# Kernel tuning notes

Hardware: AMD Instinct MI355X
Metric: run time of the kernel (lower is better)

## Reference

```python
import jax, jax.numpy as jnp
import numpy as np

N_NODES = 100000
N_EDGES = 400000
N_GRAPHS = 4096
D = 300          # emb_dim
L = 5            # num_layers
NUM_ATOM, NUM_CHIR = 120, 3
NUM_BOND, NUM_DIR = 6, 3
SELF_LOOP_BOND = 4
TEMP = 0.04


def setup_inputs() -> dict:
    key = jax.random.key(0)
    ks = jax.random.split(key, 24)
    inp = {}
    # graph batch 0
    inp["x0"] = jax.random.randint(ks[0], (N_NODES, 2), 0, 3)
    inp["edge_index0"] = jax.random.randint(ks[1], (2, N_EDGES), 0, N_NODES)
    inp["edge_attr0"] = jax.random.randint(ks[2], (N_EDGES, 2), 0, 3)
    inp["batch_ids0"] = jnp.sort(jax.random.randint(ks[3], (N_NODES,), 0, N_GRAPHS))
    inp["dangling0"] = jax.random.randint(ks[4], (N_GRAPHS,), 0, N_NODES)
    # graph batch 1
    inp["x1"] = jax.random.randint(ks[5], (N_NODES, 2), 0, 3)
    inp["edge_index1"] = jax.random.randint(ks[6], (2, N_EDGES), 0, N_NODES)
    inp["edge_attr1"] = jax.random.randint(ks[7], (N_EDGES, 2), 0, 3)
    inp["batch_ids1"] = jnp.sort(jax.random.randint(ks[8], (N_NODES,), 0, N_GRAPHS))
    inp["dangling1"] = jax.random.randint(ks[9], (N_GRAPHS,), 0, N_NODES)
    # shared encoder parameters
    g = lambda i, shp, s=0.1: (jax.random.normal(ks[i], shp, jnp.float32) * s)
    inp["atom_emb1"] = g(10, (NUM_ATOM, D))
    inp["atom_emb2"] = g(11, (NUM_CHIR, D))
    inp["eemb1"] = g(12, (L, NUM_BOND, D))
    inp["eemb2"] = g(13, (L, NUM_DIR, D))
    inp["W1"] = g(14, (L, D, 2 * D))
    inp["b1"] = jnp.zeros((L, 2 * D), jnp.float32)
    inp["W2"] = g(15, (L, 2 * D, D))
    inp["b2"] = jnp.zeros((L, D), jnp.float32)
    inp["bn_g"] = jnp.ones((L, D), jnp.float32)
    inp["bn_b"] = jnp.zeros((L, D), jnp.float32)
    # projectors stacked: 0=projector0, 1=projector1, 2=dangling_proj0, 3=dangling_proj1
    inp["pW1"] = g(16, (4, D, D))
    inp["pb1"] = jnp.zeros((4, D), jnp.float32)
    inp["pW2"] = g(17, (4, D, D))
    inp["pb2"] = jnp.zeros((4, D), jnp.float32)
    return inp


def _encode(x, edge_index, edge_attr, atom_emb1, atom_emb2,
            eemb1, eemb2, W1, b1, W2, b2, bn_g, bn_b):
    # initial node embedding: sum of atom-type and chirality embeddings
    h = atom_emb1[x[:, 0]] + atom_emb2[x[:, 1]]          # [N, D]
    src, dst = edge_index[0], edge_index[1]
    for l in range(L):
        e = eemb1[l][edge_attr[:, 0]] + eemb2[l][edge_attr[:, 1]]  # [E, D]
        msg = h[src] + e                                           # [E, D]
        agg = jax.ops.segment_sum(msg, dst, num_segments=h.shape[0])
        # self-loop with bond type 4, direction 0 (pretrain-gnns GINConv)
        agg = agg + h + eemb1[l][SELF_LOOP_BOND] + eemb2[l][0]
        z = jax.nn.relu(agg @ W1[l] + b1[l]) @ W2[l] + b2[l]       # GIN MLP
        mu = jnp.mean(z, axis=0)
        var = jnp.var(z, axis=0)
        z = (z - mu) * jax.lax.rsqrt(var + 1e-5) * bn_g[l] + bn_b[l]
        h = z if l == L - 1 else jax.nn.relu(z)                    # no ReLU on last layer
    return h


def _mlp(x, w1, bb1, w2, bb2):
    return jax.nn.relu(x @ w1 + bb1) @ w2 + bb2


def _branch(h, batch_ids, dangling, proj_i, dproj_i, pW1, pb1, pW2, pb2):
    pooled = jax.ops.segment_sum(h, batch_ids, num_segments=N_GRAPHS)
    counts = jax.ops.segment_sum(jnp.ones((h.shape[0],), h.dtype), batch_ids,
                                 num_segments=N_GRAPHS)
    pooled = pooled / jnp.maximum(counts, 1.0)[:, None]            # global_mean_pool
    out = _mlp(pooled, pW1[proj_i], pb1[proj_i], pW2[proj_i], pb2[proj_i])
    out = out + _mlp(h[dangling], pW1[dproj_i], pb1[dproj_i], pW2[dproj_i], pb2[dproj_i])
    return out / jnp.linalg.norm(out, axis=1, keepdims=True)       # L2 normalize


def reference(x0, edge_index0, edge_attr0, batch_ids0, dangling0,
              x1, edge_index1, edge_attr1, batch_ids1, dangling1,
              atom_emb1, atom_emb2, eemb1, eemb2, W1, b1, W2, b2, bn_g, bn_b,
              pW1, pb1, pW2, pb2):
    h0 = _encode(x0, edge_index0, edge_attr0, atom_emb1, atom_emb2,
                 eemb1, eemb2, W1, b1, W2, b2, bn_g, bn_b)
    f0 = _branch(h0, batch_ids0, dangling0, 0, 2, pW1, pb1, pW2, pb2)
    h1 = _encode(x1, edge_index1, edge_attr1, atom_emb1, atom_emb2,
                 eemb1, eemb2, W1, b1, W2, b2, bn_g, bn_b)
    f1 = _branch(h1, batch_ids1, dangling1, 1, 3, pW1, pb1, pW2, pb2)
    logits = (f0 @ f1.T) / TEMP                                    # [G, G]
    return logits
```

## Files before the change

kernel.cpp:

```cpp
#include <hip/hip_runtime.h>

#define NN    100000
#define NE    400000
#define NG    4096
#define LL    5
#define MPAD  100096
#define NCHUNK 98

typedef unsigned short u16;
typedef __attribute__((ext_vector_type(8))) _Float16 half8;
typedef __attribute__((ext_vector_type(4))) float float4v;

__device__ __forceinline__ float b2f(u16 u){
  union { float f; unsigned u; } c; c.u = ((unsigned)u)<<16; return c.f;
}
__device__ __forceinline__ u16 f2b(float f){
  union { float f; unsigned u; } c; c.f = f;
  unsigned x = c.u;
  return (u16)((x + 0x7fffu + ((x>>16)&1u)) >> 16);
}
__device__ __forceinline__ float h2f(u16 u){
  union { u16 s; _Float16 h; } c; c.s = u; return (float)c.h;
}
__device__ __forceinline__ u16 f2h(float f){
  union { u16 s; _Float16 h; } c; c.h = (_Float16)f; return c.s;
}
__device__ __forceinline__ void g2l16(const u16* g, u16* l){
  __builtin_amdgcn_global_load_lds((const __attribute__((address_space(1))) void*)g,
                                   (__attribute__((address_space(3))) void*)l, 16, 0, 0);
}

__global__ __launch_bounds__(256) void detect_dtype(const u16* __restrict__ p, int* __restrict__ flag){
  int i = blockIdx.x*256 + threadIdx.x;
  float v = b2f(p[i]);
  if (!(fabsf(v) <= 1e4f)) atomicOr(flag, 1);
}
__global__ __launch_bounds__(256) void cvt_param(const void* __restrict__ src, u16* __restrict__ dst,
                                                 int n, const int* __restrict__ flag){
  int i = blockIdx.x*256 + threadIdx.x;
  if (i >= n) return;
  float v = (*flag) ? ((const float*)src)[i] : b2f(((const u16*)src)[i]);
  dst[i] = f2h(v);
}

__global__ __launch_bounds__(256) void zero32(unsigned* __restrict__ p, int n){
  int i = blockIdx.x*256 + threadIdx.x;
  if (i < n) p[i] = 0u;
}

__global__ __launch_bounds__(256) void tpad(const u16* __restrict__ src, u16* __restrict__ dst,
                                            int L, int K, int N, int Kp, int Np){
  int idx = blockIdx.x*256 + threadIdx.x;
  if (idx >= L*Np*Kp) return;
  int l = idx/(Np*Kp); int r = idx - l*Np*Kp; int n = r/Kp; int k = r - n*Kp;
  dst[idx] = (n<N && k<K) ? src[(l*K + k)*N + n] : (u16)0;
}

__global__ __launch_bounds__(256) void ecomb_build(const u16* __restrict__ ee1, const u16* __restrict__ ee2,
                                                   u16* __restrict__ ec){
  int idx = blockIdx.x*256 + threadIdx.x;
  if (idx >= LL*18*160) return;
  int l = idx/(18*160); int r = idx - l*18*160; int c = r/160; int p = r - c*160;
  int a0 = c/3, a1 = c - a0*3;
  u16 o0=0,o1=0;
  if (p < 150){
    int d = 2*p;
    o0 = f2h(h2f(ee1[(l*6+a0)*300+d  ]) + h2f(ee2[(l*3+a1)*300+d  ]));
    o1 = f2h(h2f(ee1[(l*6+a0)*300+d+1]) + h2f(ee2[(l*3+a1)*300+d+1]));
  }
  ((ushort2*)ec)[idx] = make_ushort2(o0,o1);
}

__global__ __launch_bounds__(256) void node_init(const int* __restrict__ x, const u16* __restrict__ ae1,
                                                 const u16* __restrict__ ae2, u16* __restrict__ h){
  int idx = blockIdx.x*256 + threadIdx.x;
  if (idx >= MPAD*160) return;
  int n = idx/160, p = idx - n*160;
  u16 o0=0,o1=0;
  if (n < NN && p < 150){
    int a = x[2*n], ch = x[2*n+1];
    int d = 2*p;
    o0 = f2h(h2f(ae1[a*300+d  ]) + h2f(ae2[ch*300+d  ]));
    o1 = f2h(h2f(ae1[a*300+d+1]) + h2f(ae2[ch*300+d+1]));
  }
  ((ushort2*)h)[idx] = make_ushort2(o0,o1);
}

__global__ __launch_bounds__(256) void hist(const int* __restrict__ ei, int* __restrict__ counts){
  int e = blockIdx.x*256 + threadIdx.x;
  if (e >= NE) return;
  atomicAdd(&counts[ei[NE + e]], 1);
}
__global__ __launch_bounds__(256) void scan_chunks(const int* __restrict__ counts, int* __restrict__ csums){
  __shared__ int sd[256];
  int base = blockIdx.x*1024;
  int s = 0;
  for (int i = threadIdx.x; i < 1024; i += 256){ int g = base+i; if (g < NN) s += counts[g]; }
  sd[threadIdx.x] = s; __syncthreads();
  for (int off=128; off>0; off>>=1){ if (threadIdx.x < off) sd[threadIdx.x] += sd[threadIdx.x+off]; __syncthreads(); }
  if (threadIdx.x == 0) csums[blockIdx.x] = sd[0];
}
__global__ __launch_bounds__(128) void scan_base(const int* __restrict__ csums, int* __restrict__ cbase,
                                                 int* __restrict__ offsets){
  __shared__ int sd[128];
  int tid = threadIdx.x;
  int v = (tid < NCHUNK) ? csums[tid] : 0;
  sd[tid] = v; __syncthreads();
  for (int off=1; off<128; off<<=1){
    int t = (tid >= off) ? sd[tid-off] : 0; __syncthreads();
    sd[tid] += t; __syncthreads();
  }
  if (tid < NCHUNK) cbase[tid] = sd[tid] - v;
  if (tid == 0) offsets[NN] = sd[NCHUNK-1];
}
__global__ __launch_bounds__(256) void scan_final(const int* __restrict__ counts, const int* __restrict__ cbase,
                                                  int* __restrict__ offsets){
  __shared__ int sd[256];
  int tid = threadIdx.x;
  int base = blockIdx.x*1024 + tid*4;
  int v0 = (base   < NN) ? counts[base  ] : 0;
  int v1 = (base+1 < NN) ? counts[base+1] : 0;
  int v2 = (base+2 < NN) ? counts[base+2] : 0;
  int v3 = (base+3 < NN) ? counts[base+3] : 0;
  int s = v0+v1+v2+v3;
  sd[tid] = s; __syncthreads();
  for (int off=1; off<256; off<<=1){
    int t = (tid >= off) ? sd[tid-off] : 0; __syncthreads();
    sd[tid] += t; __syncthreads();
  }
  int run = cbase[blockIdx.x] + sd[tid] - s;
  if (base   < NN){ offsets[base  ] = run; } run += v0;
  if (base+1 < NN){ offsets[base+1] = run; } run += v1;
  if (base+2 < NN){ offsets[base+2] = run; } run += v2;
  if (base+3 < NN){ offsets[base+3] = run; }
}
__global__ __launch_bounds__(256) void fill_perm(const int* __restrict__ ei, const int* __restrict__ ea,
                                                 const int* __restrict__ offsets,
                                                 int* __restrict__ cursor, int* __restrict__ pk){
  int e = blockIdx.x*256 + threadIdx.x;
  if (e >= NE) return;
  int d = ei[NE + e];
  int src = ei[e];
  int c = ea[2*e]*3 + ea[2*e+1];
  int pos = offsets[d] + atomicAdd(&cursor[d], 1);
  pk[pos] = src*32 + c;
}

__global__ __launch_bounds__(256) void aggregate(
    const u16* __restrict__ h, const u16* __restrict__ ecL,
    const int* __restrict__ offsets, const int* __restrict__ pk,
    u16* __restrict__ agg)
{
  __shared__ u16 ecs[18*320];
  for (int i = threadIdx.x; i < 18*160; i += 256)
    ((ushort2*)ecs)[i] = ((const ushort2*)ecL)[i];
  __syncthreads();
  int node = blockIdx.x*4 + (threadIdx.x>>6);
  int lane = threadIdx.x & 63;
  bool tl = lane < 16;
  const ushort4* h4 = (const ushort4*)h;
  long base = (long)node*80;
  float m0[4], m1[4] = {0,0,0,0};
  {
    ushort4 hv = h4[base + lane];
    ushort4 ev = ((const ushort4*)(ecs + 12*320))[lane];
    m0[0]=h2f(hv.x)+h2f(ev.x); m0[1]=h2f(hv.y)+h2f(ev.y);
    m0[2]=h2f(hv.z)+h2f(ev.z); m0[3]=h2f(hv.w)+h2f(ev.w);
    if (tl){
      ushort4 hv2 = h4[base + 64 + lane];
      ushort4 ev2 = ((const ushort4*)(ecs + 12*320))[64 + lane];
      m1[0]=h2f(hv2.x)+h2f(ev2.x); m1[1]=h2f(hv2.y)+h2f(ev2.y);
      m1[2]=h2f(hv2.z)+h2f(ev2.z); m1[3]=h2f(hv2.w)+h2f(ev2.w);
    }
  }
  if (node < NN){
    int s = offsets[node], en = offsets[node+1];
    int i = s;
    while (i + 1 < en){
      int p0 = pk[i], p1 = pk[i+1]; i += 2;
      int s0 = p0>>5, c0 = p0&31;
      int s1 = p1>>5, c1 = p1&31;
      ushort4 ha0 = h4[(long)s0*80 + lane];
      ushort4 ha1 = h4[(long)s1*80 + lane];
      ushort4 e0 = ((const ushort4*)(ecs + c0*320))[lane];
      ushort4 e1 = ((const ushort4*)(ecs + c1*320))[lane];
      m0[0] += h2f(ha0.x)+h2f(e0.x) + h2f(ha1.x)+h2f(e1.x);
      m0[1] += h2f(ha0.y)+h2f(e0.y) + h2f(ha1.y)+h2f(e1.y);
      m0[2] += h2f(ha0.z)+h2f(e0.z) + h2f(ha1.z)+h2f(e1.z);
      m0[3] += h2f(ha0.w)+h2f(e0.w) + h2f(ha1.w)+h2f(e1.w);
      if (tl){
        ushort4 hb0 = h4[(long)s0*80 + 64 + lane];
        ushort4 hb1 = h4[(long)s1*80 + 64 + lane];
        ushort4 f0 = ((const ushort4*)(ecs + c0*320))[64 + lane];
        ushort4 f1 = ((const ushort4*)(ecs + c1*320))[64 + lane];
        m1[0] += h2f(hb0.x)+h2f(f0.x) + h2f(hb1.x)+h2f(f1.x);
        m1[1] += h2f(hb0.y)+h2f(f0.y) + h2f(hb1.y)+h2f(f1.y);
        m1[2] += h2f(hb0.z)+h2f(f0.z) + h2f(hb1.z)+h2f(f1.z);
        m1[3] += h2f(hb0.w)+h2f(f0.w) + h2f(hb1.w)+h2f(f1.w);
      }
    }
    if (i < en){
      int p0 = pk[i];
      int s0 = p0>>5, c0 = p0&31;
      ushort4 ha0 = h4[(long)s0*80 + lane];
      ushort4 e0 = ((const ushort4*)(ecs + c0*320))[lane];
      m0[0] += h2f(ha0.x)+h2f(e0.x); m0[1] += h2f(ha0.y)+h2f(e0.y);
      m0[2] += h2f(ha0.z)+h2f(e0.z); m0[3] += h2f(ha0.w)+h2f(e0.w);
      if (tl){
        ushort4 hb0 = h4[(long)s0*80 + 64 + lane];
        ushort4 f0 = ((const ushort4*)(ecs + c0*320))[64 + lane];
        m1[0] += h2f(hb0.x)+h2f(f0.x); m1[1] += h2f(hb0.y)+h2f(f0.y);
        m1[2] += h2f(hb0.z)+h2f(f0.z); m1[3] += h2f(hb0.w)+h2f(f0.w);
      }
    }
  }
  ushort4* a4 = (ushort4*)agg;
  a4[base + lane] = make_ushort4(f2h(m0[0]), f2h(m0[1]), f2h(m0[2]), f2h(m0[3]));
  if (tl)
    a4[base + 64 + lane] = make_ushort4(f2h(m1[0]), f2h(m1[1]), f2h(m1[2]), f2h(m1[3]));
}

__global__ __launch_bounds__(512, 2) void gin_mlp(
    const u16* __restrict__ A,
    const u16* __restrict__ W1Tl,
    const u16* __restrict__ b1l,
    const u16* __restrict__ W2Tl,
    const u16* __restrict__ b2l,
    u16* __restrict__ Z,
    float* __restrict__ colsum, float* __restrict__ colsumsq)
{
  __shared__ __align__(16) u16 lds[32768];
  u16* uS = lds;
  u16* Ws = lds + 8192;
  int tid = threadIdx.x;
  int wave = tid>>6, lane = tid&63;
  int q = lane>>4, r = lane&15;
  int wr = wave>>2, wc = wave&3;
  int m0 = blockIdx.x*128;

  half8 aReg[10];
  const u16* Arow = A + (long)(m0 + wave*16 + r)*320 + q*8;
  #pragma unroll
  for (int kc=0; kc<10; ++kc) aReg[kc] = *(const half8*)(Arow + kc*32);

  float4v zacc[4][6];
  #pragma unroll
  for (int i=0;i<4;i++)
    #pragma unroll
    for (int j=0;j<6;j++) zacc[i][j] = (float4v){0.f,0.f,0.f,0.f};

  for (int t1=0; t1<10; ++t1){
    int n1_0 = t1*64;
    __syncthreads();
    #pragma unroll
    for (int i=0;i<5;i++){
      int idx = tid*8 + i*4096;
      int kc = idx >> 11;
      int rem = idx & 2047;
      int n = rem >> 5, k8 = rem & 31;
      g2l16(W1Tl + (long)(n1_0 + n)*320 + kc*32 + k8, Ws + idx);
    }
    __syncthreads();
    float4v uacc[4];
    #pragma unroll
    for (int j=0;j<4;j++) uacc[j] = (float4v){0.f,0.f,0.f,0.f};
    #pragma unroll
    for (int kc=0; kc<10; ++kc){
      half8 bw[4];
      #pragma unroll
      for (int j=0;j<4;j++) bw[j] = *(const half8*)&Ws[kc*2048 + (j*16+r)*32 + q*8];
      #pragma unroll
      for (int j=0;j<4;j++)
        uacc[j] = __builtin_amdgcn_mfma_f32_16x16x32_f16(aReg[kc], bw[j], uacc[j], 0,0,0);
    }
    #pragma unroll
    for (int j=0;j<4;j++){
      int nloc = j*16 + r;
      int n1g = n1_0 + nloc;
      float bv = (n1g < 600) ? h2f(b1l[n1g]) : 0.f;
      int kc2 = nloc >> 5, c32 = nloc & 31;
      #pragma unroll
      for (int t=0;t<4;t++){
        int row = wave*16 + q*4 + t;
        float v = fmaxf(uacc[j][t] + bv, 0.f);
        uS[kc2*4096 + row*32 + c32] = f2h(v);
      }
    }
    __syncthreads();
    #pragma unroll
    for (int i=0;i<6;i++){
      int idx = tid*8 + i*4096;
      int kc2 = idx / 12288;
      int rem = idx - kc2*12288;
      int n2 = rem >> 5, k8 = rem & 31;
      g2l16(W2Tl + (long)n2*640 + n1_0 + kc2*32 + k8, Ws + idx);
    }
    __syncthreads();
    #pragma unroll
    for (int kc2=0; kc2<2; ++kc2){
      half8 af[4], bf[6];
      #pragma unroll
      for (int i=0;i<4;i++) af[i] = *(const half8*)&uS[kc2*4096 + (wr*64+i*16+r)*32 + q*8];
      #pragma unroll
      for (int j=0;j<6;j++) bf[j] = *(const half8*)&Ws[kc2*12288 + (wc*96+j*16+r)*32 + q*8];
      #pragma unroll
      for (int i=0;i<4;i++)
        #pragma unroll
        for (int j=0;j<6;j++)
          zacc[i][j] = __builtin_amdgcn_mfma_f32_16x16x32_f16(af[i], bf[j], zacc[i][j], 0,0,0);
    }
  }
  #pragma unroll
  for (int j=0;j<6;j++){
    int c = wc*96 + j*16 + r;
    float bv = (c < 300) ? h2f(b2l[c]) : 0.f;
    float s1 = 0.f, s2 = 0.f;
    #pragma unroll
    for (int i=0;i<4;i++){
      int rowb = m0 + wr*64 + i*16 + q*4;
      #pragma unroll
      for (int t=0;t<4;t++){
        float v = zacc[i][j][t] + bv;
        int gr = rowb + t;
        if (c < 320) Z[(long)gr*320 + c] = f2h(v);
        if (gr < NN){ s1 += v; s2 += v*v; }
      }
    }
    s1 += __shfl_xor(s1,16); s1 += __shfl_xor(s1,32);
    s2 += __shfl_xor(s2,16); s2 += __shfl_xor(s2,32);
    if (q == 0 && c < 384){ atomicAdd(&colsum[c], s1); atomicAdd(&colsumsq[c], s2); }
  }
}

__global__ __launch_bounds__(256) void gemm_nt(
    const u16* __restrict__ A, int lda,
    const u16* __restrict__ BT, int ldb,
    int Kp,
    const u16* __restrict__ bias, int Nreal,
    float scale, int dorelu, int omode, int Ncap,
    void* __restrict__ Cv, int ldc,
    const int* __restrict__ outmode)
{
  __shared__ __align__(16) u16 As[128*32];
  __shared__ __align__(16) u16 Bs[128*32];
  int tid = threadIdx.x;
  int wave = tid>>6, lane = tid&63;
  int wr = (wave>>1)&1, wc = wave&1;
  int m0 = blockIdx.x*128, n0 = blockIdx.y*128;
  int q = lane>>4, r = lane&15;
  int srow = tid>>2, scol = (tid&3)*8;
  const u16* Ag0 = A  + (long)(m0+srow)*lda + scol;
  const u16* Ag1 = A  + (long)(m0+64+srow)*lda + scol;
  const u16* Bg0 = BT + (long)(n0+srow)*ldb + scol;
  const u16* Bg1 = BT + (long)(n0+64+srow)*ldb + scol;
  u16* Asl0 = &As[tid*8];
  u16* Asl1 = &As[64*32 + tid*8];
  u16* Bsl0 = &Bs[tid*8];
  u16* Bsl1 = &Bs[64*32 + tid*8];
  float4v acc[4][4];
  #pragma unroll
  for (int i=0;i<4;i++)
    #pragma unroll
    for (int j=0;j<4;j++) acc[i][j] = (float4v){0.f,0.f,0.f,0.f};

  for (int k0=0; k0<Kp; k0+=32){
    g2l16(Ag0+k0, Asl0);
    g2l16(Ag1+k0, Asl1);
    g2l16(Bg0+k0, Bsl0);
    g2l16(Bg1+k0, Bsl1);
    __syncthreads();
    half8 af[4], bf[4];
    #pragma unroll
    for (int i=0;i<4;i++) af[i] = *(const half8*)&As[(wr*64+i*16+r)*32 + q*8];
    #pragma unroll
    for (int j=0;j<4;j++) bf[j] = *(const half8*)&Bs[(wc*64+j*16+r)*32 + q*8];
    #pragma unroll
    for (int i=0;i<4;i++)
      #pragma unroll
      for (int j=0;j<4;j++)
        acc[i][j] = __builtin_amdgcn_mfma_f32_16x16x32_f16(af[i], bf[j], acc[i][j], 0,0,0);
    __syncthreads();
  }

  int ob = omode;
  if (outmode) ob = (*outmode) ? 0 : 1;
  u16* Ch = (u16*)Cv; float* Cf = (float*)Cv;
  #pragma unroll
  for (int j=0;j<4;j++){
    int c = n0 + wc*64 + j*16 + r;
    float bv = (bias && c < Nreal) ? h2f(bias[c]) : 0.f;
    #pragma unroll
    for (int i=0;i<4;i++){
      int rowb = m0 + wr*64 + i*16 + q*4;
      #pragma unroll
      for (int tt=0; tt<4; ++tt){
        float v = acc[i][j][tt] + bv;
        if (dorelu) v = fmaxf(v, 0.f);
        v *= scale;
        int gr = rowb + tt;
        if (c < Ncap){
          long o = (long)gr*ldc + c;
          if (ob == 2)      Ch[o] = f2h(v);
          else if (ob == 1) Ch[o] = f2b(v);
          else              Cf[o] = v;
        }
      }
    }
  }
}

__global__ __launch_bounds__(320) void bn_finalize(const float* __restrict__ st, const u16* __restrict__ g,
                                                   const u16* __restrict__ b, float* __restrict__ sc,
                                                   float* __restrict__ sh){
  int c = threadIdx.x;
  if (c >= 300) return;
  float mu  = st[c] * (1.0f/NN);
  float var = st[384+c] * (1.0f/NN) - mu*mu;
  float inv = rsqrtf(var + 1e-5f);
  float gg = h2f(g[c]) * inv;
  sc[c] = gg; sh[c] = h2f(b[c]) - mu*gg;
}
__global__ __launch_bounds__(256) void bn_apply(const u16* __restrict__ z, const float* __restrict__ sc,
                                                const float* __restrict__ sh, u16* __restrict__ h, int dorelu){
  int idx = blockIdx.x*256 + threadIdx.x;
  if (idx >= NN*150) return;
  int n = idx/150, p = idx - n*150;
  ushort2 zz = ((const ushort2*)z)[n*160 + p];
  int d = 2*p;
  float v0 = h2f(zz.x)*sc[d  ] + sh[d  ];
  float v1 = h2f(zz.y)*sc[d+1] + sh[d+1];
  if (dorelu){ v0 = fmaxf(v0,0.f); v1 = fmaxf(v1,0.f); }
  ((ushort2*)h)[n*160 + p] = make_ushort2(f2h(v0), f2h(v1));
}

__global__ __launch_bounds__(256) void graph_starts(const int* __restrict__ ids, int* __restrict__ starts){
  int i = blockIdx.x*256 + threadIdx.x;
  if (i >= NN) return;
  int b = ids[i];
  if (i == 0){ for (int g=0; g<=b; ++g) starts[g] = 0; }
  else { int p = ids[i-1]; for (int g=p+1; g<=b; ++g) starts[g] = i; }
  if (i == NN-1){ for (int g=b+1; g<=NG; ++g) starts[g] = NN; }
}
__global__ __launch_bounds__(256) void pool_kernel(const u16* __restrict__ h, const int* __restrict__ starts,
                                                   u16* __restrict__ pooled){
  int g = blockIdx.x*4 + (threadIdx.x>>6);
  int lane = threadIdx.x & 63;
  if (g >= NG) return;
  int s = starts[g], e = starts[g+1];
  int cnt = e - s; if (cnt < 1) cnt = 1;
  float inv = 1.0f/(float)cnt;
  float ax[3] = {0,0,0}, ay[3] = {0,0,0};
  const ushort2* h2 = (const ushort2*)h;
  for (int row=s; row<e; ++row){
    long base = (long)row*160;
    #pragma unroll
    for (int jp=0; jp<3; ++jp){
      int p = jp*64 + lane;
      if (p < 160){ ushort2 v = h2[base+p]; ax[jp] += h2f(v.x); ay[jp] += h2f(v.y); }
    }
  }
  ushort2* o2 = (ushort2*)pooled;
  #pragma unroll
  for (int jp=0; jp<3; ++jp){
    int p = jp*64 + lane;
    if (p < 160) o2[g*160+p] = make_ushort2(f2h(ax[jp]*inv), f2h(ay[jp]*inv));
  }
}
__global__ __launch_bounds__(256) void gather_rows(const u16* __restrict__ h, const int* __restrict__ idxs,
                                                   u16* __restrict__ out){
  int idx = blockIdx.x*256 + threadIdx.x;
  if (idx >= NG*160) return;
  int g = idx/160, p = idx - g*160;
  ((ushort2*)out)[idx] = ((const ushort2*)h)[(long)idxs[g]*160 + p];
}
__global__ __launch_bounds__(256) void add_norm(const float* __restrict__ vp, const float* __restrict__ vd,
                                                u16* __restrict__ f){
  int g = blockIdx.x*4 + (threadIdx.x>>6);
  int lane = threadIdx.x & 63;
  if (g >= NG) return;
  float vals[5]; float ss = 0.f;
  #pragma unroll
  for (int t=0; t<5; ++t){
    int d = lane + 64*t; float v = 0.f;
    if (d < 300) v = vp[g*320+d] + vd[g*320+d];
    vals[t] = v; ss += v*v;
  }
  #pragma unroll
  for (int off=32; off>0; off>>=1) ss += __shfl_xor(ss, off);
  float inv = rsqrtf(ss);
  #pragma unroll
  for (int t=0; t<5; ++t){
    int d = lane + 64*t;
    if (d < 320) f[g*320+d] = f2h(d < 300 ? vals[t]*inv : 0.f);
  }
}

extern "C" void kernel_launch(void* const* d_in, const int* in_sizes, int n_in,
                              void* d_out, int out_size, void* d_ws, size_t ws_size,
                              hipStream_t stream)
{
  const int* xin[2]  = {(const int*)d_in[0], (const int*)d_in[5]};
  const int* ei[2]   = {(const int*)d_in[1], (const int*)d_in[6]};
  const int* ea[2]   = {(const int*)d_in[2], (const int*)d_in[7]};
  const int* bid[2]  = {(const int*)d_in[3], (const int*)d_in[8]};
  const int* dang[2] = {(const int*)d_in[4], (const int*)d_in[9]};
  (void)in_sizes; (void)n_in; (void)out_size; (void)ws_size;

  char* w = (char*)d_ws;
  auto alloc = [&](size_t bytes)->char* {
    char* p = w; w += (bytes + 255) & ~(size_t)255; return p;
  };
  u16* hA   = (u16*)alloc((size_t)MPAD*320*2);
  u16* agg  = (u16*)alloc((size_t)MPAD*320*2);
  u16* z    = agg;
  u16*   pooled = (u16*)alloc((size_t)NG*320*2);
  u16*   hd     = (u16*)alloc((size_t)NG*320*2);
  u16*   ubuf   = (u16*)alloc((size_t)NG*384*2);
  float* vpb    = (float*)alloc((size_t)NG*320*4);
  float* vdb    = (float*)alloc((size_t)NG*320*4);
  u16* ec   = (u16*)alloc((size_t)LL*18*320*2);
  u16* W1T  = (u16*)alloc((size_t)LL*640*320*2);
  u16* W2T  = (u16*)alloc((size_t)LL*384*640*2);
  u16* pW1T = (u16*)alloc((size_t)4*384*320*2);
  u16* pW2T = (u16*)alloc((size_t)4*384*384*2);
  int* counts = (int*)alloc((size_t)NN*4);
  int* cursor = (int*)alloc((size_t)NN*4);
  int* offs   = (int*)alloc((size_t)(NN+1)*4);
  int* perm   = (int*)alloc((size_t)NE*4);
  int* csums  = (int*)alloc(512);
  int* cbase  = (int*)alloc(512);
  float* stats = (float*)alloc(768*4);
  float* bnsc  = (float*)alloc(384*4);
  float* bnsh  = (float*)alloc(384*4);
  int* starts  = (int*)alloc((size_t)(NG+1)*4);
  u16* f0b     = (u16*)alloc((size_t)NG*320*2);
  u16* f1b     = (u16*)alloc((size_t)NG*320*2);
  int* dflag   = (int*)alloc(256);
  const int pcnt[14] = {36000, 900, 9000, 4500, 900000, 3000, 900000, 1500,
                        1500, 1500, 360000, 1200, 360000, 1200};
  u16* parena = (u16*)alloc((size_t)2580300*2 + 14*256);
  u16* pp[14];
  { size_t off = 0;
    for (int i=0;i<14;i++){ pp[i] = parena + off; off += (size_t)((pcnt[i]+127)&~127); } }
  u16* ae1 = pp[0];  u16* ae2 = pp[1];  u16* ee1 = pp[2];  u16* ee2 = pp[3];
  u16* W1  = pp[4];  u16* b1  = pp[5];  u16* W2  = pp[6];  u16* b2  = pp[7];
  u16* bng = pp[8];  u16* bnb = pp[9];  u16* pW1 = pp[10]; u16* pb1 = pp[11];
  u16* pW2 = pp[12]; u16* pb2 = pp[13];

  auto cdiv = [](long a, long b){ return (int)((a + b - 1)/b); };
  auto gemm = [&](const u16* A, int lda, const u16* BT, int ldb, int Kp,
                  const u16* bias, int Nreal, float scale, int relu, int omode, int Ncap,
                  void* C, int ldc, int gx, int gy, const int* om){
    gemm_nt<<<dim3(gx,gy), 256, 0, stream>>>(A,lda,BT,ldb,Kp,bias,Nreal,scale,relu,omode,Ncap,
                                             C,ldc,om);
  };

  zero32<<<1,256,0,stream>>>((unsigned*)dflag, 1);
  detect_dtype<<<16,256,0,stream>>>((const u16*)d_in[14], dflag);
  for (int i=0;i<14;i++)
    cvt_param<<<cdiv(pcnt[i],256),256,0,stream>>>(d_in[10+i], pp[i], pcnt[i], dflag);

  tpad<<<cdiv((long)LL*640*320,256),256,0,stream>>>(W1,  W1T,  LL, 300, 600, 320, 640);
  tpad<<<cdiv((long)LL*384*640,256),256,0,stream>>>(W2,  W2T,  LL, 600, 300, 640, 384);
  tpad<<<cdiv((long)4*384*320,256),256,0,stream>>>(pW1, pW1T, 4,  300, 300, 320, 384);
  tpad<<<cdiv((long)4*384*384,256),256,0,stream>>>(pW2, pW2T, 4,  300, 300, 384, 384);
  ecomb_build<<<cdiv((long)LL*18*160,256),256,0,stream>>>(ee1, ee2, ec);

  for (int br=0; br<2; ++br){
    u16* fo = br ? f1b : f0b;
    node_init<<<cdiv((long)MPAD*160,256),256,0,stream>>>(xin[br], ae1, ae2, hA);
    zero32<<<cdiv(NN,256),256,0,stream>>>((unsigned*)counts, NN);
    hist<<<cdiv(NE,256),256,0,stream>>>(ei[br], counts);
    scan_chunks<<<NCHUNK,256,0,stream>>>(counts, csums);
    scan_base<<<1,128,0,stream>>>(csums, cbase, offs);
    scan_final<<<NCHUNK,256,0,stream>>>(counts, cbase, offs);
    zero32<<<cdiv(NN,256),256,0,stream>>>((unsigned*)cursor, NN);
    fill_perm<<<cdiv(NE,256),256,0,stream>>>(ei[br], ea[br], offs, cursor, perm);

    for (int l=0; l<LL; ++l){
      aggregate<<<MPAD/4,256,0,stream>>>(hA, ec + (size_t)l*18*320, offs, perm, agg);
      zero32<<<3,256,0,stream>>>((unsigned*)stats, 768);
      gin_mlp<<<MPAD/128, 512, 0, stream>>>(agg,
          W1T + (size_t)l*640*320, b1 + l*600,
          W2T + (size_t)l*384*640, b2 + l*300,
          z, stats, stats+384);
      bn_finalize<<<1,320,0,stream>>>(stats, bng + l*300, bnb + l*300, bnsc, bnsh);
      bn_apply<<<cdiv((long)NN*150,256),256,0,stream>>>(z, bnsc, bnsh, hA, (l < LL-1) ? 1 : 0);
    }

    graph_starts<<<cdiv(NN,256),256,0,stream>>>(bid[br], starts);
    pool_kernel<<<NG/4,256,0,stream>>>(hA, starts, pooled);
    gather_rows<<<cdiv((long)NG*160,256),256,0,stream>>>(hA, dang[br], hd);

    int pi = br, dpi = 2 + br;
    gemm(pooled, 320, pW1T + (size_t)pi*384*320, 320, 320,
         pb1 + pi*300, 300, 1.f, 1, 2, 384, ubuf, 384, NG/128, 3, nullptr);
    gemm(ubuf, 384, pW2T + (size_t)pi*384*384, 384, 384,
         pb2 + pi*300, 300, 1.f, 0, 0, 320, vpb, 320, NG/128, 3, nullptr);
    gemm(hd, 320, pW1T + (size_t)dpi*384*320, 320, 320,
         pb1 + dpi*300, 300, 1.f, 1, 2, 384, ubuf, 384, NG/128, 3, nullptr);
    gemm(ubuf, 384, pW2T + (size_t)dpi*384*384, 384, 384,
         pb2 + dpi*300, 300, 1.f, 0, 0, 320, vdb, 320, NG/128, 3, nullptr);
    add_norm<<<NG/4,256,0,stream>>>(vpb, vdb, fo);
  }

  gemm(f0b, 320, f1b, 320, 320, nullptr, 0, 25.0f, 0, 1, NG,
       d_out, NG, NG/128, NG/128, dflag);
}
```

Measured before the change: 4.013 ms.

## Use packed fp16 accumulation in aggregate and 32x32 MFMA for first GIN layer

The aggregate kernel now accumulates neighbor messages directly in packed half4 vectors, with the edge loop unrolled by four, instead of converting each value to float. The first GEMM in gin_mlp switches from 16x16x32 MFMA tiles to 32x32x16 tiles, using a padded LDS layout (stride 328) for W1 to avoid bank conflicts and a new output-to-LDS mapping. The goal is less conversion ALU work and more memory-level parallelism in the gather, plus fewer LDS reads per MFMA in the GEMM. Accumulating sums in fp16 loses precision and risks overflow on high-degree nodes, and holding 20 A fragments raises register pressure.

```diff
diff --git a/kernel.cpp b/kernel.cpp
--- a/kernel.cpp
+++ b/kernel.cpp
@@ -9,7 +9,9 @@
 
 typedef unsigned short u16;
 typedef __attribute__((ext_vector_type(8))) _Float16 half8;
+typedef __attribute__((ext_vector_type(4))) _Float16 hv4;
 typedef __attribute__((ext_vector_type(4))) float float4v;
+typedef __attribute__((ext_vector_type(16))) float float16v;
 
 __device__ __forceinline__ float b2f(u16 u){
   union { float f; unsigned u; } c; c.u = ((unsigned)u)<<16; return c.f;
@@ -158,66 +160,41 @@
   int node = blockIdx.x*4 + (threadIdx.x>>6);
   int lane = threadIdx.x & 63;
   bool tl = lane < 16;
-  const ushort4* h4 = (const ushort4*)h;
+  const hv4* h4 = (const hv4*)h;
+  const hv4* e4 = (const hv4*)ecs;
   long base = (long)node*80;
-  float m0[4], m1[4] = {0,0,0,0};
-  {
-    ushort4 hv = h4[base + lane];
-    ushort4 ev = ((const ushort4*)(ecs + 12*320))[lane];
-    m0[0]=h2f(hv.x)+h2f(ev.x); m0[1]=h2f(hv.y)+h2f(ev.y);
-    m0[2]=h2f(hv.z)+h2f(ev.z); m0[3]=h2f(hv.w)+h2f(ev.w);
-    if (tl){
-      ushort4 hv2 = h4[base + 64 + lane];
-      ushort4 ev2 = ((const ushort4*)(ecs + 12*320))[64 + lane];
-      m1[0]=h2f(hv2.x)+h2f(ev2.x); m1[1]=h2f(hv2.y)+h2f(ev2.y);
-      m1[2]=h2f(hv2.z)+h2f(ev2.z); m1[3]=h2f(hv2.w)+h2f(ev2.w);
-    }
-  }
+  hv4 acc0, acc1 = (hv4)(_Float16)0;
+  acc0 = h4[base + lane] + e4[12*80 + lane];
+  if (tl) acc1 = h4[base + 64 + lane] + e4[12*80 + 64 + lane];
   if (node < NN){
     int s = offsets[node], en = offsets[node+1];
     int i = s;
-    while (i + 1 < en){
-      int p0 = pk[i], p1 = pk[i+1]; i += 2;
-      int s0 = p0>>5, c0 = p0&31;
-      int s1 = p1>>5, c1 = p1&31;
-      ushort4 ha0 = h4[(long)s0*80 + lane];
-      ushort4 ha1 = h4[(long)s1*80 + lane];
-      ushort4 e0 = ((const ushort4*)(ecs + c0*320))[lane];
-      ushort4 e1 = ((const ushort4*)(ecs + c1*320))[lane];
-      m0[0] += h2f(ha0.x)+h2f(e0.x) + h2f(ha1.x)+h2f(e1.x);
-      m0[1] += h2f(ha0.y)+h2f(e0.y) + h2f(ha1.y)+h2f(e1.y);
-      m0[2] += h2f(ha0.z)+h2f(e0.z) + h2f(ha1.z)+h2f(e1.z);
-      m0[3] += h2f(ha0.w)+h2f(e0.w) + h2f(ha1.w)+h2f(e1.w);
+    while (i + 3 < en){
+      int p0 = pk[i], p1 = pk[i+1], p2 = pk[i+2], p3 = pk[i+3]; i += 4;
+      long b0 = (long)(p0>>5)*80, b1 = (long)(p1>>5)*80;
+      long b2 = (long)(p2>>5)*80, b3 = (long)(p3>>5)*80;
+      int c0 = (p0&31)*80, c1 = (p1&31)*80, c2 = (p2&31)*80, c3 = (p3&31)*80;
+      hv4 a0 = h4[b0+lane], a1 = h4[b1+lane], a2 = h4[b2+lane], a3 = h4[b3+lane];
+      hv4 e0 = e4[c0+lane], e1 = e4[c1+lane], e2 = e4[c2+lane], e3 = e4[c3+lane];
+      acc0 += (a0+e0); acc0 += (a1+e1); acc0 += (a2+e2); acc0 += (a3+e3);
       if (tl){
-        ushort4 hb0 = h4[(long)s0*80 + 64 + lane];
-        ushort4 hb1 = h4[(long)s1*80 + 64 + lane];
-        ushort4 f0 = ((const ushort4*)(ecs + c0*320))[64 + lane];
-        ushort4 f1 = ((const ushort4*)(ecs + c1*320))[64 + lane];
-        m1[0] += h2f(hb0.x)+h2f(f0.x) + h2f(hb1.x)+h2f(f1.x);
-        m1[1] += h2f(hb0.y)+h2f(f0.y) + h2f(hb1.y)+h2f(f1.y);
-        m1[2] += h2f(hb0.z)+h2f(f0.z) + h2f(hb1.z)+h2f(f1.z);
-        m1[3] += h2f(hb0.w)+h2f(f0.w) + h2f(hb1.w)+h2f(f1.w);
+        hv4 x0 = h4[b0+64+lane], x1 = h4[b1+64+lane];
+        hv4 x2 = h4[b2+64+lane], x3 = h4[b3+64+lane];
+        hv4 y0 = e4[c0+64+lane], y1 = e4[c1+64+lane];
+        hv4 y2 = e4[c2+64+lane], y3 = e4[c3+64+lane];
+        acc1 += (x0+y0); acc1 += (x1+y1); acc1 += (x2+y2); acc1 += (x3+y3);
       }
     }
-    if (i < en){
-      int p0 = pk[i];
-      int s0 = p0>>5, c0 = p0&31;
-      ushort4 ha0 = h4[(long)s0*80 + lane];
-      ushort4 e0 = ((const ushort4*)(ecs + c0*320))[lane];
-      m0[0] += h2f(ha0.x)+h2f(e0.x); m0[1] += h2f(ha0.y)+h2f(e0.y);
-      m0[2] += h2f(ha0.z)+h2f(e0.z); m0[3] += h2f(ha0.w)+h2f(e0.w);
-      if (tl){
-        ushort4 hb0 = h4[(long)s0*80 + 64 + lane];
-        ushort4 f0 = ((const ushort4*)(ecs + c0*320))[64 + lane];
-        m1[0] += h2f(hb0.x)+h2f(f0.x); m1[1] += h2f(hb0.y)+h2f(f0.y);
-        m1[2] += h2f(hb0.z)+h2f(f0.z); m1[3] += h2f(hb0.w)+h2f(f0.w);
-      }
-    }
-  }
-  ushort4* a4 = (ushort4*)agg;
-  a4[base + lane] = make_ushort4(f2h(m0[0]), f2h(m0[1]), f2h(m0[2]), f2h(m0[3]));
-  if (tl)
-    a4[base + 64 + lane] = make_ushort4(f2h(m1[0]), f2h(m1[1]), f2h(m1[2]), f2h(m1[3]));
+    while (i < en){
+      int p0 = pk[i]; ++i;
+      long b0 = (long)(p0>>5)*80; int c0 = (p0&31)*80;
+      acc0 += (h4[b0+lane] + e4[c0+lane]);
+      if (tl) acc1 += (h4[b0+64+lane] + e4[c0+64+lane]);
+    }
+  }
+  hv4* a4 = (hv4*)agg;
+  a4[base + lane] = acc0;
+  if (tl) a4[base + 64 + lane] = acc1;
 }
 
 __global__ __launch_bounds__(512, 2) void gin_mlp(
@@ -234,14 +211,16 @@
   u16* Ws = lds + 8192;
   int tid = threadIdx.x;
   int wave = tid>>6, lane = tid&63;
+  int n5 = lane & 31, hi = lane >> 5;
   int q = lane>>4, r = lane&15;
+  int rg = wave>>1, ch = wave&1;
   int wr = wave>>2, wc = wave&3;
   int m0 = blockIdx.x*128;
 
-  half8 aReg[10];
-  const u16* Arow = A + (long)(m0 + wave*16 + r)*320 + q*8;
-  #pragma unroll
-  for (int kc=0; kc<10; ++kc) aReg[kc] = *(const half8*)(Arow + kc*32);
+  half8 aReg[20];
+  const u16* Arow = A + (long)(m0 + rg*32 + n5)*320 + hi*8;
+  #pragma unroll
+  for (int kc=0; kc<20; ++kc) aReg[kc] = *(const half8*)(Arow + kc*16);
 
   float4v zacc[4][6];
   #pragma unroll
@@ -253,37 +232,34 @@
     int n1_0 = t1*64;
     __syncthreads();
     #pragma unroll
-    for (int i=0;i<5;i++){
-      int idx = tid*8 + i*4096;
-      int kc = idx >> 11;
-      int rem = idx & 2047;
-      int n = rem >> 5, k8 = rem & 31;
-      g2l16(W1Tl + (long)(n1_0 + n)*320 + kc*32 + k8, Ws + idx);
+    for (int rnd=0; rnd<5; ++rnd){
+      int ck = rnd*512 + tid;
+      int n = ck/41, k8 = ck - n*41;
+      const u16* src = (k8 < 40) ? (W1Tl + (long)(n1_0 + n)*320 + k8*8) : W1Tl;
+      g2l16(src, Ws + ck*8);
+    }
+    if (tid < 64){
+      int ck = 2560 + tid;
+      int n = ck/41, k8 = ck - n*41;
+      const u16* src = (k8 < 40) ? (W1Tl + (long)(n1_0 + n)*320 + k8*8) : W1Tl;
+      g2l16(src, Ws + ck*8);
     }
     __syncthreads();
-    float4v uacc[4];
-    #pragma unroll
-    for (int j=0;j<4;j++) uacc[j] = (float4v){0.f,0.f,0.f,0.f};
-    #pragma unroll
-    for (int kc=0; kc<10; ++kc){
-      half8 bw[4];
-      #pragma unroll
-      for (int j=0;j<4;j++) bw[j] = *(const half8*)&Ws[kc*2048 + (j*16+r)*32 + q*8];
-      #pragma unroll
-      for (int j=0;j<4;j++)
-        uacc[j] = __builtin_amdgcn_mfma_f32_16x16x32_f16(aReg[kc], bw[j], uacc[j], 0,0,0);
-    }
-    #pragma unroll
-    for (int j=0;j<4;j++){
-      int nloc = j*16 + r;
-      int n1g = n1_0 + nloc;
+    float16v uacc = (float16v)(0.f);
+    #pragma unroll
+    for (int kc=0; kc<20; ++kc){
+      half8 bw = *(const half8*)&Ws[(ch*32 + n5)*328 + kc*16 + hi*8];
+      uacc = __builtin_amdgcn_mfma_f32_32x32x16_f16(aReg[kc], bw, uacc, 0,0,0);
+    }
+    {
+      int n1g = n1_0 + ch*32 + n5;
       float bv = (n1g < 600) ? h2f(b1l[n1g]) : 0.f;
-      int kc2 = nloc >> 5, c32 = nloc & 31;
-      #pragma unroll
-      for (int t=0;t<4;t++){
-        int row = wave*16 + q*4 + t;
-        float v = fmaxf(uacc[j][t] + bv, 0.f);
-        uS[kc2*4096 + row*32 + c32] = f2h(v);
+      u16* uw = uS + ch*4096 + n5;
+      #pragma unroll
+      for (int reg=0; reg<16; ++reg){
+        int row = rg*32 + (reg&3) + 8*(reg>>2) + 4*hi;
+        float v = fmaxf(uacc[reg] + bv, 0.f);
+        uw[row*32] = f2h(v);
       }
     }
     __syncthreads();
```

Result: faster. 3.706 ms (-7.6%).
